# Kernel tuning notes

Measured on AMD Instinct MI355X. Metric: run time of the kernel, lower is better.

Reference implementation:

```python
import jax, jax.numpy as jnp
import numpy as np

SR = 22050
FRAME_LENGTH = 64
ATTENUATE_GAIN = 0.02


def upsample_linear(x, scale):
    """torch nn.Upsample(mode='linear', align_corners=False) along last axis."""
    T = x.shape[-1]
    S = T * scale
    # source coordinate for each output sample (half-pixel convention), clamped
    coords = jnp.clip((jnp.arange(S, dtype=jnp.float32) + 0.5) / scale - 0.5, 0.0, T - 1)
    i0 = jnp.floor(coords).astype(jnp.int32)
    i1 = jnp.minimum(i0 + 1, T - 1)
    w = (coords - i0).astype(x.dtype)
    return x[..., i0] * (1.0 - w) + x[..., i1] * w


def setup_inputs() -> dict:
    key = jax.random.key(0)
    k1, k2, k3 = jax.random.split(key, 3)
    B, T, P, STR = 16, 1000, 64, 6
    # fundamental frequencies in [50, 450] Hz so high partials hit the Nyquist mask
    six_f0 = jax.random.uniform(k1, (B, T, STR), dtype=jnp.float32) * 400.0 + 50.0
    c = jax.random.uniform(k2, (STR, B, P, T), dtype=jnp.float32)
    a = jax.random.uniform(k3, (STR, B, T), dtype=jnp.float32)
    return {"six_f0": six_f0, "c": c, "a": a, "string_idx": 1}


def reference(six_f0, c, a, string_idx):
    sidx = string_idx - 1
    fundamentals = six_f0[..., sidx]        # (B, T)
    c_bank = c[sidx]                        # (B, P, T)
    loudness = a[sidx]                      # (B, T)
    P = c_bank.shape[1]

    partial_mult = jnp.arange(1, P + 1, dtype=jnp.float32)[:, None]   # (P, 1)
    f0_bank = fundamentals[:, None, :] * partial_mult                  # (B, P, T)
    mask = (f0_bank < SR / 2).astype(c_bank.dtype)
    c_masked = c_bank * mask

    f0_up = upsample_linear(f0_bank, FRAME_LENGTH)                     # (B, P, S)
    phase = jnp.cumsum(f0_up / SR, axis=2)
    a_up = upsample_linear(c_masked, FRAME_LENGTH)                     # (B, P, S)
    sinusoid_bank = jnp.sin(2.0 * np.pi * phase) * a_up * ATTENUATE_GAIN

    loudness_up = upsample_linear(loudness, FRAME_LENGTH)              # (B, S)
    return jnp.sum(sinusoid_bank, axis=1) * loudness_up                # (B, S)
```

## Files before the change

### kernel.cpp

```cpp
#include <hip/hip_runtime.h>
#include <math.h>

constexpr int B = 16, T = 1000, P = 64, STR = 6, SCALE = 64;
constexpr int S = T * SCALE;
constexpr int SEG_PITCH = 1024;
#define NYQ 11025.0f
#define INV_SR (1.0f / 22050.0f)

__device__ __forceinline__ float fracf_(float x) {
#if __has_builtin(__builtin_amdgcn_fractf)
  return __builtin_amdgcn_fractf(x);
#else
  return x - floorf(x);
#endif
}

__device__ __forceinline__ float sin2pi(float r) {
#if __has_builtin(__builtin_amdgcn_sinf)
  return __builtin_amdgcn_sinf(r);
#else
  return __sinf(r * 6.28318530717958647692f);
#endif
}

__global__ __launch_bounds__(256) void k_segbase(
    const float* __restrict__ six_f0, const int* __restrict__ sidx_p,
    float* __restrict__ segbase) {
  const int b = blockIdx.x;
  const int tid = threadIdx.x;
  const int sidx = sidx_p[0] - 1;

  __shared__ float Fs[T];
  for (int t = tid; t < T; t += 256)
    Fs[t] = six_f0[(size_t)(b * T + t) * STR + sidx];
  __syncthreads();

  double loc[4];
  double run = 0.0;
#pragma unroll
  for (int j = 0; j < 4; ++j) {
    int g = 4 * tid + j;
    double ssum = 0.0;
    if (g == 0)
      ssum = 32.0 * (double)Fs[0];
    else if (g <= T - 1)
      ssum = 32.0 * ((double)Fs[g - 1] + (double)Fs[g]);
    else if (g == T)
      ssum = 32.0 * (double)Fs[T - 1];
    loc[j] = run;
    run += ssum;
  }

  const int lane = tid & 63, wid = tid >> 6;
  double v = run;
  for (int off = 1; off < 64; off <<= 1) {
    double n = __shfl_up(v, off, 64);
    if (lane >= off) v += n;
  }
  __shared__ double wtot[4];
  if (lane == 63) wtot[wid] = v;
  __syncthreads();
  double excl = v - run;
  for (int w = 0; w < wid; ++w) excl += wtot[w];

#pragma unroll
  for (int j = 0; j < 4; ++j) {
    int g = 4 * tid + j;
    if (g <= T) {
      double ph = (excl + loc[j]) / 22050.0;
      ph -= floor(ph);
      segbase[b * SEG_PITCH + g] = (float)ph;
    }
  }
}

__global__ __launch_bounds__(256) void k_synth(
    const float* __restrict__ six_f0, const float* __restrict__ c,
    const float* __restrict__ a, const int* __restrict__ sidx_p,
    const float* __restrict__ segbase, float* __restrict__ out) {
  const int b = blockIdx.y;
  const int s0 = blockIdx.x * 256;
  const int tid = threadIdx.x;
  const int sidx = sidx_p[0] - 1;
  const float* cb = c + (size_t)sidx * B * P * T;
  const float* loud = a + (size_t)sidx * B * T + (size_t)b * T;

  const int g0 = (s0 + 32) >> 6;
  const int g3 = (s0 + 255 + 32) >> 6;
  const int fmin = max(g0 - 1, 0);
  const int fmax = min(g3, T - 1);
  const int nf = fmax - fmin + 1;

  __shared__ float Fsh[8];
  __shared__ float amps[8][64];

  if (tid < nf)
    Fsh[tid] = six_f0[(size_t)(b * T + fmin + tid) * STR + sidx];
  __syncthreads();

  for (int i = tid; i < 512; i += 256) {
    int p = i >> 3, f = i & 7;
    if (f < nf) {
      float cv = cb[((size_t)b * P + p) * T + fmin + f];
      float F = Fsh[f];
      amps[f][p] = ((float)(p + 1) * F < NYQ) ? cv : 0.0f;
    }
  }
  __syncthreads();

  const int s = s0 + tid;
  const int g = (s + 32) >> 6;
  const int lo = (g == 0) ? 0 : (g - 1);
  const int hi = min(g, T - 1);
  const int segstart = (g == 0) ? 0 : ((g << 6) - 32);
  const int k = s - segstart;
  const float kf1 = (float)(k + 1);

  const float Flo = Fsh[lo - fmin];
  const float Fhi = Fsh[hi - fmin];
  const float base = segbase[b * SEG_PITCH + g];
  const float local =
      (kf1 * Flo + (Fhi - Flo) * kf1 * kf1 * (1.0f / 128.0f)) * INV_SR;
  const float phi = fracf_(base + local);
  const float w = ((float)k + 0.5f) * (1.0f / 64.0f);
  const float l0 = loud[lo];
  const float lup = l0 + w * (loud[hi] - l0);

  const float Fmn = fminf(Flo, Fhi);
  const int pmax = min(P, (int)(NYQ / Fmn) + 1);

  const int lo_l = lo - fmin, hi_l = hi - fmin;
  float acc = 0.0f, pf = 1.0f;
#pragma unroll 4
  for (int p = 0; p < pmax; ++p) {
    float a0 = amps[lo_l][p];
    float a1 = amps[hi_l][p];
    float amp = a0 + w * (a1 - a0);
    float r = fracf_(pf * phi);
    acc = fmaf(sin2pi(r), amp, acc);
    pf += 1.0f;
  }
  out[(size_t)b * S + s] = acc * 0.02f * lup;
}

extern "C" void kernel_launch(void* const* d_in, const int* in_sizes, int n_in,
                              void* d_out, int out_size, void* d_ws,
                              size_t ws_size, hipStream_t stream) {
  const float* six_f0 = (const float*)d_in[0];
  const float* c = (const float*)d_in[1];
  const float* a = (const float*)d_in[2];
  const int* sidx = (const int*)d_in[3];
  float* out = (float*)d_out;
  float* segbase = (float*)d_ws;

  hipLaunchKernelGGL(k_segbase, dim3(B), dim3(256), 0, stream, six_f0, sidx,
                     segbase);
  hipLaunchKernelGGL(k_synth, dim3(S / 256, B), dim3(256), 0, stream, six_f0,
                     c, a, sidx, segbase, out);
}
```

Baseline: 94.82 us.

## Use Chebyshev sine recurrence across partials with 4 samples per thread

The synthesis inner loop drops the per-partial fract and hardware sine. It instead generates sin(p*phi) with the recurrence s_{p+1} = 2cos(phi)*s_p - s_{p-1}, seeded by one sin and one cos per sample. Each thread now computes 4 consecutive samples sharing one segment, so amplitude loads from a transposed, padded shared array are reused across the 4 samples, and output is written with float4 stores. Blocks cover 16 frame segments, with loudness staged in shared memory. The recurrence can accumulate float error over up to 64 partials.

New measurement: 87.30 us. -7.9%, faster.

```diff
diff --git a/kernel.cpp b/kernel.cpp
--- a/kernel.cpp
+++ b/kernel.cpp
@@ -4,6 +4,9 @@
 constexpr int B = 16, T = 1000, P = 64, STR = 6, SCALE = 64;
 constexpr int S = T * SCALE;
 constexpr int SEG_PITCH = 1024;
+constexpr int SEGS_PER_BLK = 16;
+constexpr int NF = 17;
+constexpr int NBLK = 63;
 #define NYQ 11025.0f
 #define INV_SR (1.0f / 22050.0f)
 
@@ -14,12 +17,18 @@
   return x - floorf(x);
 #endif
 }
-
 __device__ __forceinline__ float sin2pi(float r) {
 #if __has_builtin(__builtin_amdgcn_sinf)
   return __builtin_amdgcn_sinf(r);
 #else
   return __sinf(r * 6.28318530717958647692f);
+#endif
+}
+__device__ __forceinline__ float cos2pi(float r) {
+#if __has_builtin(__builtin_amdgcn_cosf)
+  return __builtin_amdgcn_cosf(r);
+#else
+  return __cosf(r * 6.28318530717958647692f);
 #endif
 }
 
@@ -79,68 +88,91 @@
     const float* __restrict__ a, const int* __restrict__ sidx_p,
     const float* __restrict__ segbase, float* __restrict__ out) {
   const int b = blockIdx.y;
-  const int s0 = blockIdx.x * 256;
+  const int G0 = blockIdx.x * SEGS_PER_BLK;
+  const int fbase = G0 - 1;
   const int tid = threadIdx.x;
   const int sidx = sidx_p[0] - 1;
   const float* cb = c + (size_t)sidx * B * P * T;
   const float* loud = a + (size_t)sidx * B * T + (size_t)b * T;
 
-  const int g0 = (s0 + 32) >> 6;
-  const int g3 = (s0 + 255 + 32) >> 6;
-  const int fmin = max(g0 - 1, 0);
-  const int fmax = min(g3, T - 1);
-  const int nf = fmax - fmin + 1;
+  __shared__ float Fsh[NF];
+  __shared__ float Lsh[NF];
+  __shared__ float ampsT[P][NF + 1];
 
-  __shared__ float Fsh[8];
-  __shared__ float amps[8][64];
-
-  if (tid < nf)
-    Fsh[tid] = six_f0[(size_t)(b * T + fmin + tid) * STR + sidx];
-  __syncthreads();
-
-  for (int i = tid; i < 512; i += 256) {
-    int p = i >> 3, f = i & 7;
-    if (f < nf) {
-      float cv = cb[((size_t)b * P + p) * T + fmin + f];
-      float F = Fsh[f];
-      amps[f][p] = ((float)(p + 1) * F < NYQ) ? cv : 0.0f;
-    }
+  if (tid < NF) {
+    int f = min(max(fbase + tid, 0), T - 1);
+    Fsh[tid] = six_f0[(size_t)(b * T + f) * STR + sidx];
+  } else if (tid < 2 * NF) {
+    int i = tid - NF;
+    int f = min(max(fbase + i, 0), T - 1);
+    Lsh[i] = loud[f];
   }
   __syncthreads();
 
-  const int s = s0 + tid;
-  const int g = (s + 32) >> 6;
-  const int lo = (g == 0) ? 0 : (g - 1);
-  const int hi = min(g, T - 1);
-  const int segstart = (g == 0) ? 0 : ((g << 6) - 32);
-  const int k = s - segstart;
-  const float kf1 = (float)(k + 1);
+  for (int i = tid; i < P * NF; i += 256) {
+    int p = i / NF, fl = i - p * NF;
+    int f = min(max(fbase + fl, 0), T - 1);
+    float F = Fsh[fl];
+    float cv = cb[((size_t)b * P + p) * T + f];
+    ampsT[p][fl] = ((float)(p + 1) * F < NYQ) ? cv : 0.0f;
+  }
+  __syncthreads();
 
-  const float Flo = Fsh[lo - fmin];
-  const float Fhi = Fsh[hi - fmin];
-  const float base = segbase[b * SEG_PITCH + g];
-  const float local =
-      (kf1 * Flo + (Fhi - Flo) * kf1 * kf1 * (1.0f / 128.0f)) * INV_SR;
-  const float phi = fracf_(base + local);
-  const float w = ((float)k + 0.5f) * (1.0f / 64.0f);
-  const float l0 = loud[lo];
-  const float lup = l0 + w * (loud[hi] - l0);
+  const int seg = G0 + (tid >> 4);
+  const int q = tid & 15;
+  const int lo_l = tid >> 4;
+  const float Flo = Fsh[lo_l];
+  const float Fhi = Fsh[lo_l + 1];
+  const float Llo = Lsh[lo_l];
+  const float dL = Lsh[lo_l + 1] - Llo;
+  const float dF = Fhi - Flo;
+  const float base = segbase[b * SEG_PITCH + min(seg, SEG_PITCH - 1)];
+  const int kadj = (seg == 0) ? -32 : 0;
+  const int kp = q * 4;
+
+  float wj[4], twoC[4], scur[4], sprev[4], accj[4];
+#pragma unroll
+  for (int j = 0; j < 4; ++j) {
+    int k = kp + j + kadj;
+    float kf1 = (float)(k + 1);
+    float local = (kf1 * Flo + dF * kf1 * kf1 * (1.0f / 128.0f)) * INV_SR;
+    float phi = fracf_(base + local);
+    wj[j] = ((float)k + 0.5f) * (1.0f / 64.0f);
+    twoC[j] = 2.0f * cos2pi(phi);
+    scur[j] = sin2pi(phi);
+    sprev[j] = 0.0f;
+    accj[j] = 0.0f;
+  }
 
   const float Fmn = fminf(Flo, Fhi);
   const int pmax = min(P, (int)(NYQ / Fmn) + 1);
 
-  const int lo_l = lo - fmin, hi_l = hi - fmin;
-  float acc = 0.0f, pf = 1.0f;
-#pragma unroll 4
+  const float* row = &ampsT[0][lo_l];
+#pragma unroll 2
   for (int p = 0; p < pmax; ++p) {
-    float a0 = amps[lo_l][p];
-    float a1 = amps[hi_l][p];
-    float amp = a0 + w * (a1 - a0);
-    float r = fracf_(pf * phi);
-    acc = fmaf(sin2pi(r), amp, acc);
-    pf += 1.0f;
+    float a0 = row[p * (NF + 1)];
+    float a1 = row[p * (NF + 1) + 1];
+    float d = a1 - a0;
+#pragma unroll
+    for (int j = 0; j < 4; ++j) {
+      float amp = fmaf(wj[j], d, a0);
+      accj[j] = fmaf(amp, scur[j], accj[j]);
+      float sn = fmaf(twoC[j], scur[j], -sprev[j]);
+      sprev[j] = scur[j];
+      scur[j] = sn;
+    }
   }
-  out[(size_t)b * S + s] = acc * 0.02f * lup;
+
+  bool live = (seg < 1000) ? !(seg == 0 && q < 8) : (seg == 1000 && q < 8);
+  if (live) {
+    int s0 = seg * 64 - 32 + kp;
+    float4 r;
+    r.x = accj[0] * 0.02f * fmaf(wj[0], dL, Llo);
+    r.y = accj[1] * 0.02f * fmaf(wj[1], dL, Llo);
+    r.z = accj[2] * 0.02f * fmaf(wj[2], dL, Llo);
+    r.w = accj[3] * 0.02f * fmaf(wj[3], dL, Llo);
+    *(float4*)(out + (size_t)b * S + s0) = r;
+  }
 }
 
 extern "C" void kernel_launch(void* const* d_in, const int* in_sizes, int n_in,
@@ -155,6 +187,6 @@
 
   hipLaunchKernelGGL(k_segbase, dim3(B), dim3(256), 0, stream, six_f0, sidx,
                      segbase);
-  hipLaunchKernelGGL(k_synth, dim3(S / 256, B), dim3(256), 0, stream, six_f0,
-                     c, a, sidx, segbase, out);
+  hipLaunchKernelGGL(k_synth, dim3(NBLK, B), dim3(256), 0, stream, six_f0, c,
+                     a, sidx, segbase, out);
 }
```
